# Performance work log

Measured on AMD Instinct MI355X. Metric: run time of the kernel, lower is better.

## Reference

```python
import jax, jax.numpy as jnp
import numpy as np

# Model config (matches init_kwargs)
V, SMAX, D, DH, H, M, L = 32000, 512, 512, 64, 8, 2048, 6
B, S, T = 4, 512, 512
PAD = 0

_SPEC = [
    ("tok_emb", (V, D), "n"), ("pos_emb", (SMAX, D), "n"),
    ("enc_ln1_w", (L, D), "1"), ("enc_ln1_b", (L, D), "0"),
    ("enc_wq", (L, H, D, DH), "n"), ("enc_wk", (L, H, D, DH), "n"), ("enc_wv", (L, H, D, DH), "n"),
    ("enc_wo", (L, H * DH, D), "n"), ("enc_bo", (L, D), "0"),
    ("enc_ln2_w", (L, D), "1"), ("enc_ln2_b", (L, D), "0"),
    ("enc_w1", (L, D, M), "n"), ("enc_b1", (L, M), "0"),
    ("enc_w2", (L, M, D), "n"), ("enc_b2", (L, D), "0"),
    ("enc_lnf_w", (D,), "1"), ("enc_lnf_b", (D,), "0"),
    ("dec_ln1_w", (L, D), "1"), ("dec_ln1_b", (L, D), "0"),
    ("dec_wq_s", (L, H, D, DH), "n"), ("dec_wk_s", (L, H, D, DH), "n"), ("dec_wv_s", (L, H, D, DH), "n"),
    ("dec_wo_s", (L, H * DH, D), "n"), ("dec_bo_s", (L, D), "0"),
    ("dec_ln2_w", (L, D), "1"), ("dec_ln2_b", (L, D), "0"),
    ("dec_wq_c", (L, H, D, DH), "n"), ("dec_wk_c", (L, H, D, DH), "n"), ("dec_wv_c", (L, H, D, DH), "n"),
    ("dec_wo_c", (L, H * DH, D), "n"), ("dec_bo_c", (L, D), "0"),
    ("dec_ln3_w", (L, D), "1"), ("dec_ln3_b", (L, D), "0"),
    ("dec_w1", (L, D, M), "n"), ("dec_b1", (L, M), "0"),
    ("dec_w2", (L, M, D), "n"), ("dec_b2", (L, D), "0"),
    ("dec_lnf_w", (D,), "1"), ("dec_lnf_b", (D,), "0"),
    ("head_w", (D, V), "n"), ("head_b", (V,), "0"),
]


def setup_inputs() -> dict:
    key = jax.random.key(0)
    k1, k2, key = jax.random.split(key, 3)
    inp = {
        "tokens_source": jax.random.randint(k1, (B, S), 0, V),
        "tokens_destination": jax.random.randint(k2, (B, T), 0, V),
    }
    for name, shape, kind in _SPEC:
        if kind == "n":
            key, k = jax.random.split(key)
            inp[name] = jax.random.normal(k, shape, jnp.float32) * 0.02
        elif kind == "1":
            inp[name] = jnp.ones(shape, jnp.float32)
        else:
            inp[name] = jnp.zeros(shape, jnp.float32)
    return inp


def _ln(x, w, b):
    mu = x.mean(-1, keepdims=True)
    var = ((x - mu) ** 2).mean(-1, keepdims=True)
    return (x - mu) * jax.lax.rsqrt(var + 1e-5) * w + b


def _mha(xq, xkv, wq, wk, wv, wo, bo, mask):
    # wq/wk/wv: [H, D, dh]; wo: [H*dh, D]; mask: bool [B or 1, Sq, Sk] (broadcast over heads)
    q = jnp.einsum("bsd,hde->bhse", xq, wq)
    k = jnp.einsum("btd,hde->bhte", xkv, wk)
    v = jnp.einsum("btd,hde->bhte", xkv, wv)
    scores = jnp.einsum("bhse,bhte->bhst", q, k) / (DH ** 0.5)
    scores = jnp.where(mask[:, None], scores, -jnp.inf)
    w = jax.nn.softmax(scores, axis=-1)
    o = jnp.einsum("bhst,bhte->bhse", w, v)
    b_, _, s_, _ = o.shape
    o = o.transpose(0, 2, 1, 3).reshape(b_, s_, H * DH)  # concat heads (head 0 first)
    return o @ wo + bo


def _forward(src, dst, p):
    s_, t_ = src.shape[1], dst.shape[1]
    key_mask = (src != PAD)[:, None, :]                      # [B,1,S]: mask over source keys
    causal = jnp.tril(jnp.ones((t_, t_), bool))[None]        # [1,T,T]
    x = p["tok_emb"][src] + p["pos_emb"][:s_]
    for i in range(L):
        h = _ln(x, p["enc_ln1_w"][i], p["enc_ln1_b"][i])
        x = x + _mha(h, h, p["enc_wq"][i], p["enc_wk"][i], p["enc_wv"][i], p["enc_wo"][i], p["enc_bo"][i], key_mask)
        h = _ln(x, p["enc_ln2_w"][i], p["enc_ln2_b"][i])
        x = x + jax.nn.gelu(h @ p["enc_w1"][i] + p["enc_b1"][i], approximate=False) @ p["enc_w2"][i] + p["enc_b2"][i]
    xe = _ln(x, p["enc_lnf_w"], p["enc_lnf_b"])
    y = p["tok_emb"][dst] + p["pos_emb"][:t_]
    for i in range(L):
        h = _ln(y, p["dec_ln1_w"][i], p["dec_ln1_b"][i])
        y = y + _mha(h, h, p["dec_wq_s"][i], p["dec_wk_s"][i], p["dec_wv_s"][i], p["dec_wo_s"][i], p["dec_bo_s"][i], causal)
        h = _ln(y, p["dec_ln2_w"][i], p["dec_ln2_b"][i])
        y = y + _mha(h, xe, p["dec_wq_c"][i], p["dec_wk_c"][i], p["dec_wv_c"][i], p["dec_wo_c"][i], p["dec_bo_c"][i], key_mask)
        h = _ln(y, p["dec_ln3_w"][i], p["dec_ln3_b"][i])
        y = y + jax.nn.gelu(h @ p["dec_w1"][i] + p["dec_b1"][i], approximate=False) @ p["dec_w2"][i] + p["dec_b2"][i]
    yd = _ln(y, p["dec_lnf_w"], p["dec_lnf_b"])
    return yd @ p["head_w"] + p["head_b"]  # logits [B, T, V]


def reference(tokens_source, tokens_destination, tok_emb, pos_emb, enc_ln1_w, enc_ln1_b, enc_wq, enc_wk, enc_wv, enc_wo, enc_bo, enc_ln2_w, enc_ln2_b, enc_w1, enc_b1, enc_w2, enc_b2, enc_lnf_w, enc_lnf_b, dec_ln1_w, dec_ln1_b, dec_wq_s, dec_wk_s, dec_wv_s, dec_wo_s, dec_bo_s, dec_ln2_w, dec_ln2_b, dec_wq_c, dec_wk_c, dec_wv_c, dec_wo_c, dec_bo_c, dec_ln3_w, dec_ln3_b, dec_w1, dec_b1, dec_w2, dec_b2, dec_lnf_w, dec_lnf_b, head_w, head_b):
    p = {k: v for k, v in locals().items() if k not in ("tokens_source", "tokens_destination")}
    return _forward(tokens_source, tokens_destination, p)
```

## Files before the change

### kernel.cpp

```cpp
#include <hip/hip_runtime.h>
#include <math.h>


typedef __bf16 bf16;
typedef bf16  bf16x8 __attribute__((ext_vector_type(8)));
typedef float f32x4  __attribute__((ext_vector_type(4)));

#define DEV __device__ __forceinline__

DEV f32x4 mfma16(bf16x8 a, bf16x8 b, f32x4 c) {
  return __builtin_amdgcn_mfma_f32_16x16x32_bf16(a, b, c, 0, 0, 0);
}

DEV void async_copy16(const bf16* g, bf16* l) {
  __builtin_amdgcn_global_load_lds(
      (__attribute__((address_space(1))) void*)(g),
      (__attribute__((address_space(3))) void*)(l), 16, 0, 0);
}

struct TJob { const float* in; bf16* out; long long oHi, oLo, oOfs; int R, C, zdiv, tile0; };
struct TJobs { TJob j[17]; };

__global__ __launch_bounds__(256) void tcast_all(TJobs JJ, int njobs)
{
  __shared__ float tile[32][33];
  const int t = blockIdx.x;
  int ji = 0;
#pragma unroll
  for (int k = 1; k < 17; ++k) if (k < njobs && JJ.j[k].tile0 <= t) ji = k;
  const TJob J = JJ.j[ji];
  const int rel  = t - J.tile0;
  const int ntx  = J.C >> 5, nty = J.R >> 5;
  const int perz = ntx * nty;
  const int z    = rel / perz;
  const int r2   = rel - z * perz;
  const int bx   = r2 % ntx, by = r2 / ntx;

  const long long zi = (long long)z * J.R * J.C;
  const long long zo = (long long)(z / J.zdiv) * J.oHi + (long long)(z % J.zdiv) * J.oLo + J.oOfs;
  const int c0 = bx * 32, r0 = by * 32;
  const int tx = threadIdx.x & 31, ty = (threadIdx.x >> 5);
#pragma unroll
  for (int i = 0; i < 32; i += 8)
    tile[ty + i][tx] = J.in[zi + (long long)(r0 + ty + i) * J.C + c0 + tx];
  __syncthreads();
#pragma unroll
  for (int i = 0; i < 32; i += 8)
    J.out[zo + (long long)(c0 + ty + i) * J.R + r0 + tx] = (bf16)tile[tx][ty + i];
}

__global__ __launch_bounds__(64) void embedln_kernel(
    const int* __restrict__ tok, const float* __restrict__ temb,
    const float* __restrict__ pemb, float* __restrict__ x,
    const float* __restrict__ w, const float* __restrict__ b,
    bf16* __restrict__ out)
{
  const int row  = blockIdx.x;
  const int sPos = row & 511;
  const int t    = tok[row];
  const int lane = threadIdx.x;
  const int c0   = lane * 8;
  f32x4 a0 = *(const f32x4*)&temb[(long long)t * 512 + c0];
  f32x4 a1 = *(const f32x4*)&temb[(long long)t * 512 + c0 + 4];
  f32x4 p0 = *(const f32x4*)&pemb[(long long)sPos * 512 + c0];
  f32x4 p1 = *(const f32x4*)&pemb[(long long)sPos * 512 + c0 + 4];
  a0 += p0; a1 += p1;
  *(f32x4*)&x[(long long)row * 512 + c0]     = a0;
  *(f32x4*)&x[(long long)row * 512 + c0 + 4] = a1;
  float s = 0.f, q = 0.f;
#pragma unroll
  for (int k = 0; k < 4; ++k) { s += a0[k] + a1[k]; q += a0[k]*a0[k] + a1[k]*a1[k]; }
#pragma unroll
  for (int m = 1; m < 64; m <<= 1) { s += __shfl_xor(s, m); q += __shfl_xor(q, m); }
  const float mean = s * (1.f / 512.f);
  const float var  = q * (1.f / 512.f) - mean * mean;
  const float rs   = rsqrtf(var + 1e-5f);
  f32x4 w0 = *(const f32x4*)&w[c0], w1 = *(const f32x4*)&w[c0 + 4];
  f32x4 b0 = *(const f32x4*)&b[c0], b1 = *(const f32x4*)&b[c0 + 4];
  bf16x8 o;
#pragma unroll
  for (int k = 0; k < 4; ++k) {
    o[k]     = (bf16)((a0[k] - mean) * rs * w0[k] + b0[k]);
    o[k + 4] = (bf16)((a1[k] - mean) * rs * w1[k] + b1[k]);
  }
  *(bf16x8*)&out[(long long)row * 512 + c0] = o;
}

__global__ __launch_bounds__(256) void addln_kernel(
    const bf16* __restrict__ g, const float* __restrict__ bias,
    float* __restrict__ x, const float* __restrict__ w,
    const float* __restrict__ bb, bf16* __restrict__ out)
{
  const int row  = blockIdx.x * 4 + (threadIdx.x >> 6);
  const int lane = threadIdx.x & 63;
  const int c0   = lane * 8;
  float* xr = x + (long long)row * 512;
  f32x4 a0 = *(const f32x4*)&xr[c0];
  f32x4 a1 = *(const f32x4*)&xr[c0 + 4];
  bf16x8 gv = *(const bf16x8*)&g[(long long)row * 512 + c0];
  f32x4 bi0 = *(const f32x4*)&bias[c0], bi1 = *(const f32x4*)&bias[c0 + 4];
  float v[8];
#pragma unroll
  for (int k = 0; k < 4; ++k) {
    v[k]     = a0[k] + (float)gv[k]     + bi0[k];
    v[k + 4] = a1[k] + (float)gv[k + 4] + bi1[k];
  }
  *(f32x4*)&xr[c0]     = f32x4{v[0], v[1], v[2], v[3]};
  *(f32x4*)&xr[c0 + 4] = f32x4{v[4], v[5], v[6], v[7]};
  float s = 0.f, q = 0.f;
#pragma unroll
  for (int k = 0; k < 8; ++k) { s += v[k]; q += v[k] * v[k]; }
#pragma unroll
  for (int m = 1; m < 64; m <<= 1) { s += __shfl_xor(s, m); q += __shfl_xor(q, m); }
  const float mean = s * (1.f / 512.f);
  const float var  = q * (1.f / 512.f) - mean * mean;
  const float rs   = rsqrtf(var + 1e-5f);
  f32x4 w0 = *(const f32x4*)&w[c0], w1 = *(const f32x4*)&w[c0 + 4];
  f32x4 b0 = *(const f32x4*)&bb[c0], b1 = *(const f32x4*)&bb[c0 + 4];
  bf16x8 o;
#pragma unroll
  for (int k = 0; k < 4; ++k) {
    o[k]     = (bf16)((v[k] - mean) * rs * w0[k] + b0[k]);
    o[k + 4] = (bf16)((v[k + 4] - mean) * rs * w1[k] + b1[k]);
  }
  *(bf16x8*)&out[(long long)row * 512 + c0] = o;
}

template <int MODE>
__global__ __launch_bounds__(64) void attn_kernel(
    const bf16* __restrict__ Q, const bf16* __restrict__ K,
    const bf16* __restrict__ Vt, bf16* __restrict__ O,
    const int* __restrict__ srctok)
{
  __shared__ bf16 Pw[16 * 68];
  const int bh = blockIdx.y;
  const int b  = bh >> 3;
  const int q0 = blockIdx.x * 16;
  const int ln = threadIdx.x;
  const int lr = ln & 15, g = ln >> 4;
  const bf16* Qg = Q + ((long long)bh * 512 + q0) * 64;
  const bf16* Kg = K + (long long)bh * 512 * 64;
  const bf16* Vg = Vt + (long long)bh * 64 * 512;
  const int* tkb = srctok + b * 512;

  const bf16x8 aq0 = *(const bf16x8*)&Qg[lr * 64 + g * 8];
  const bf16x8 aq1 = *(const bf16x8*)&Qg[lr * 64 + 32 + g * 8];

  float m[4] = {-1e30f, -1e30f, -1e30f, -1e30f};
  float l[4] = {0.f, 0.f, 0.f, 0.f};
  f32x4 o[4] = {};

  const int ktEnd = (MODE == 1) ? (q0 + 16) : 512;
  for (int kt = 0; kt < ktEnd; kt += 64) {
    f32x4 sf[4] = {};
#pragma unroll
    for (int j = 0; j < 4; ++j) {
      const bf16x8 bk0 = *(const bf16x8*)&Kg[(long long)(kt + j * 16 + lr) * 64 + g * 8];
      const bf16x8 bk1 = *(const bf16x8*)&Kg[(long long)(kt + j * 16 + lr) * 64 + 32 + g * 8];
      sf[j] = mfma16(aq0, bk0, sf[j]);
      sf[j] = mfma16(aq1, bk1, sf[j]);
    }
    float rm[4] = {-1e30f, -1e30f, -1e30f, -1e30f};
#pragma unroll
    for (int j = 0; j < 4; ++j) {
      if (MODE == 0) {
        const bool ok = (tkb[kt + j * 16 + lr] != 0);
#pragma unroll
        for (int r = 0; r < 4; ++r) if (!ok) sf[j][r] = -1e30f;
      } else {
        const int key = kt + j * 16 + lr;
#pragma unroll
        for (int r = 0; r < 4; ++r)
          if (key > q0 + g * 4 + r) sf[j][r] = -1e30f;
      }
#pragma unroll
      for (int r = 0; r < 4; ++r) rm[r] = fmaxf(rm[r], sf[j][r]);
    }
#pragma unroll
    for (int mk = 1; mk < 16; mk <<= 1)
#pragma unroll
      for (int r = 0; r < 4; ++r) rm[r] = fmaxf(rm[r], __shfl_xor(rm[r], mk));
    float al[4], ps[4] = {0.f, 0.f, 0.f, 0.f};
#pragma unroll
    for (int r = 0; r < 4; ++r) {
      const float mx = fmaxf(m[r], rm[r]);
      al[r] = __expf(m[r] - mx);
      m[r] = mx;
    }
#pragma unroll
    for (int j = 0; j < 4; ++j) {
#pragma unroll
      for (int r = 0; r < 4; ++r) {
        const float p = (sf[j][r] <= -1e29f) ? 0.f : __expf(sf[j][r] - m[r]);
        ps[r] += p;
        Pw[(g * 4 + r) * 68 + j * 16 + lr] = (bf16)p;
      }
    }
#pragma unroll
    for (int mk = 1; mk < 16; mk <<= 1)
#pragma unroll
      for (int r = 0; r < 4; ++r) ps[r] += __shfl_xor(ps[r], mk);
#pragma unroll
    for (int r = 0; r < 4; ++r) l[r] = l[r] * al[r] + ps[r];
#pragma unroll
    for (int n = 0; n < 4; ++n)
#pragma unroll
      for (int r = 0; r < 4; ++r) o[n][r] *= al[r];
#pragma unroll
    for (int ks = 0; ks < 2; ++ks) {
      const bf16x8 ap = *(const bf16x8*)&Pw[lr * 68 + ks * 32 + g * 8];
#pragma unroll
      for (int n = 0; n < 4; ++n) {
        const bf16x8 bv = *(const bf16x8*)&Vg[(long long)(n * 16 + lr) * 512 + kt + ks * 32 + g * 8];
        o[n] = mfma16(ap, bv, o[n]);
      }
    }
  }

#pragma unroll
  for (int r = 0; r < 4; ++r) {
    const float inv = 1.f / l[r];
    const long long gr = (long long)b * 512 + q0 + g * 4 + r;
#pragma unroll
    for (int n = 0; n < 4; ++n)
      O[gr * 512 + (bh & 7) * 64 + n * 16 + lr] = (bf16)(o[n][r] * inv);
  }
}

template <int BM, int BN, int EPI, bool SWZ = false>
__global__ __launch_bounds__(256) void gemm_kernel(
    const bf16* __restrict__ A, const bf16* __restrict__ Bw,
    void* __restrict__ Cc, const float* __restrict__ bias,
    const int K, const int lda, const int ldb, const int ldc,
    const long long sAz, const long long sBz,
    const long long sClo, const long long sChi, const int HB,
    const float scale)
{
  constexpr int BK = 64;
  __shared__ bf16 As[BM * BK];
  __shared__ bf16 Bs[BN * BK];
  constexpr int AISS = (BM * BK * 2) / 4096;
  constexpr int BISS = (BN * BK * 2) / 4096;

  const int z = blockIdx.z;
  const bf16* Az = A + (long long)z * sAz;
  const bf16* Bz = Bw + (long long)z * sBz;
  const long long cofs = (long long)(z % HB) * sClo + (long long)(z / HB) * sChi;

  const int tid  = threadIdx.x;
  const int wave = tid >> 6;
  const int lane = tid & 63;
  const int lr   = lane & 15;
  const int kg   = lane >> 4;

  int bx = blockIdx.x, by = blockIdx.y;
  if constexpr (SWZ) {
    const int nx = gridDim.x;
    const int nwg = nx * gridDim.y;
    const int id = by * nx + bx;
    const int chunk = nwg >> 3;
    const int swz = (id & 7) * chunk + (id >> 3);
    bx = swz % nx; by = swz / nx;
  }
  const int m0 = bx * BM;
  const int n0 = by * BN;

  constexpr int FM = BM / 32;
  constexpr int FN = BN / 32;
  const int wm = (wave >> 1) * (BM / 2);
  const int wn = (wave & 1) * (BN / 2);

  f32x4 acc[FM][FN] = {};

  for (int kt = 0; kt < K; kt += BK) {
#pragma unroll
    for (int i = 0; i < AISS; ++i) {
      const int o = i * 4096 + tid * 16;
      const int r = o >> 7;
      const int c = (o & 127) >> 1;
      async_copy16(Az + (long long)(m0 + r) * lda + kt + c, (bf16*)((char*)As + o));
    }
#pragma unroll
    for (int i = 0; i < BISS; ++i) {
      const int o = i * 4096 + tid * 16;
      const int r = o >> 7;
      const int c = (o & 127) >> 1;
      async_copy16(Bz + (long long)(n0 + r) * ldb + kt + c, (bf16*)((char*)Bs + o));
    }
    __syncthreads();
#pragma unroll
    for (int ks = 0; ks < 2; ++ks) {
      bf16x8 af[FM], bq[FN];
#pragma unroll
      for (int i = 0; i < FM; ++i)
        af[i] = *(const bf16x8*)&As[(wm + i * 16 + lr) * BK + ks * 32 + kg * 8];
#pragma unroll
      for (int j = 0; j < FN; ++j)
        bq[j] = *(const bf16x8*)&Bs[(wn + j * 16 + lr) * BK + ks * 32 + kg * 8];
#pragma unroll
      for (int i = 0; i < FM; ++i)
#pragma unroll
        for (int j = 0; j < FN; ++j)
          acc[i][j] = mfma16(af[i], bq[j], acc[i][j]);
    }
    __syncthreads();
  }

#pragma unroll
  for (int i = 0; i < FM; ++i) {
#pragma unroll
    for (int j = 0; j < FN; ++j) {
      const int gc = n0 + wn + j * 16 + lr;
#pragma unroll
      for (int r = 0; r < 4; ++r) {
        const int gr = m0 + wm + i * 16 + kg * 4 + r;
        const float v = acc[i][j][r];
        if constexpr (EPI == 0) {
          ((bf16*)Cc + cofs)[(long long)gr * ldc + gc] = (bf16)v;
        } else if constexpr (EPI == 3) {
          float t = v + bias[gc];
          t = 0.5f * t * (1.f + erff(t * 0.70710678118654752f));
          ((bf16*)Cc)[(long long)gr * ldc + gc] = (bf16)t;
        } else if constexpr (EPI == 4) {
          __builtin_nontemporal_store(v + bias[gc], &((float*)Cc)[(long long)gr * ldc + gc]);
        } else if constexpr (EPI == 7) {
          const int sel = gc >> 9;
          const int hh = (gc >> 6) & 7, ee = gc & 63;
          const int bb = gr >> 9, ss = gr & 511;
          bf16* base = (bf16*)Cc + (long long)sel * (2048 * 512);
          const float vv = (sel == 0) ? v * 0.125f : v;
          if (sel < 2) base[(((long long)(bb * 8 + hh) << 9) + ss) * 64 + ee] = (bf16)vv;
          else         base[(((long long)(bb * 8 + hh) << 6) + ee) * 512 + ss] = (bf16)vv;
        } else if constexpr (EPI == 8) {
          const int sel = gc >> 9;
          const int hh = (gc >> 6) & 7, ee = gc & 63;
          const int bb = gr >> 9, ss = gr & 511;
          bf16* base = (bf16*)Cc + (long long)z * sChi + (long long)sel * (2048 * 512);
          if (sel == 0) base[(((long long)(bb * 8 + hh) << 9) + ss) * 64 + ee] = (bf16)v;
          else          base[(((long long)(bb * 8 + hh) << 6) + ee) * 512 + ss] = (bf16)v;
        }
      }
    }
  }
}

extern "C" void kernel_launch(void* const* d_in, const int* in_sizes, int n_in,
                              void* d_out, int out_size, void* d_ws, size_t ws_size,
                              hipStream_t stream)
{
  const int*   tok_src   = (const int*)d_in[0];
  const int*   tok_dst   = (const int*)d_in[1];
  const float* tok_emb   = (const float*)d_in[2];
  const float* pos_emb   = (const float*)d_in[3];
  const float* enc_ln1_w = (const float*)d_in[4];
  const float* enc_ln1_b = (const float*)d_in[5];
  const float* enc_wq    = (const float*)d_in[6];
  const float* enc_wk    = (const float*)d_in[7];
  const float* enc_wv    = (const float*)d_in[8];
  const float* enc_wo    = (const float*)d_in[9];
  const float* enc_bo    = (const float*)d_in[10];
  const float* enc_ln2_w = (const float*)d_in[11];
  const float* enc_ln2_b = (const float*)d_in[12];
  const float* enc_w1    = (const float*)d_in[13];
  const float* enc_b1    = (const float*)d_in[14];
  const float* enc_w2    = (const float*)d_in[15];
  const float* enc_b2    = (const float*)d_in[16];
  const float* enc_lnf_w = (const float*)d_in[17];
  const float* enc_lnf_b = (const float*)d_in[18];
  const float* dec_ln1_w = (const float*)d_in[19];
  const float* dec_ln1_b = (const float*)d_in[20];
  const float* dec_wq_s  = (const float*)d_in[21];
  const float* dec_wk_s  = (const float*)d_in[22];
  const float* dec_wv_s  = (const float*)d_in[23];
  const float* dec_wo_s  = (const float*)d_in[24];
  const float* dec_bo_s  = (const float*)d_in[25];
  const float* dec_ln2_w = (const float*)d_in[26];
  const float* dec_ln2_b = (const float*)d_in[27];
  const float* dec_wq_c  = (const float*)d_in[28];
  const float* dec_wk_c  = (const float*)d_in[29];
  const float* dec_wv_c  = (const float*)d_in[30];
  const float* dec_wo_c  = (const float*)d_in[31];
  const float* dec_bo_c  = (const float*)d_in[32];
  const float* dec_ln3_w = (const float*)d_in[33];
  const float* dec_ln3_b = (const float*)d_in[34];
  const float* dec_w1    = (const float*)d_in[35];
  const float* dec_b1    = (const float*)d_in[36];
  const float* dec_w2    = (const float*)d_in[37];
  const float* dec_b2    = (const float*)d_in[38];
  const float* dec_lnf_w = (const float*)d_in[39];
  const float* dec_lnf_b = (const float*)d_in[40];
  const float* head_w    = (const float*)d_in[41];
  const float* head_b    = (const float*)d_in[42];
  float* outp = (float*)d_out;

  char* wp = (char*)d_ws;
  auto alloc = [&](size_t nbytes) -> char* {
    char* p = wp; wp += (nbytes + 255) & ~(size_t)255; return p;
  };
  const long long LQKV = 1536LL * 512;
  const long long LKV  = 1024LL * 512;
  const long long LSQ  = 512LL * 512;
  const long long LFF  = 2048LL * 512;
  const long long KVST = 2LL * 2048 * 512;

  bf16* tQKV_e = (bf16*)alloc((size_t)6 * LQKV * 2);
  bf16* tQKV_s = (bf16*)alloc((size_t)6 * LQKV * 2);
  bf16* tQ_c   = (bf16*)alloc((size_t)6 * LSQ * 2);
  bf16* tKV_c  = (bf16*)alloc((size_t)6 * LKV * 2);
  bf16* tWo_e  = (bf16*)alloc((size_t)6 * LSQ * 2);
  bf16* tWo_s  = (bf16*)alloc((size_t)6 * LSQ * 2);
  bf16* tWo_c  = (bf16*)alloc((size_t)6 * LSQ * 2);
  bf16* tW1_e  = (bf16*)alloc((size_t)6 * LFF * 2);
  bf16* tW2_e  = (bf16*)alloc((size_t)6 * LFF * 2);
  bf16* tW1_d  = (bf16*)alloc((size_t)6 * LFF * 2);
  bf16* tW2_d  = (bf16*)alloc((size_t)6 * LFF * 2);
  bf16* tHead  = (bf16*)alloc((size_t)32000 * 512 * 2);

  float* x   = (float*)alloc((size_t)2048 * 512 * 4);
  float* y   = (float*)alloc((size_t)2048 * 512 * 4);
  bf16*  h   = (bf16*)alloc((size_t)2048 * 512 * 2);
  bf16*  qkv = (bf16*)alloc((size_t)3 * 2048 * 512 * 2);
  bf16*  xe  = (bf16*)alloc((size_t)2048 * 512 * 2);
  bf16*  kvc = (bf16*)alloc((size_t)6 * KVST * 2);
  bf16*  ob  = (bf16*)alloc((size_t)2048 * 512 * 2);
  bf16*  t0  = (bf16*)alloc((size_t)2048 * 512 * 2);
  bf16*  h1  = (bf16*)alloc((size_t)2048 * 2048 * 2);
  bf16*  yd  = (bf16*)alloc((size_t)2048 * 512 * 2);

  bf16* ql = qkv;
  bf16* kl = qkv + 2048 * 512;
  bf16* vt = qkv + 2 * 2048 * 512;

  TJobs JJ; int nt = 0, nj = 0;
  auto addjob = [&](const float* in, bf16* out, int R, int C,
                    long long oHi, long long oLo, int zdiv, long long oOfs, int nz) {
    JJ.j[nj] = TJob{in, out, oHi, oLo, oOfs, R, C, zdiv, nt};
    nt += (C / 32) * (R / 32) * nz; ++nj;
  };
  addjob(enc_wq,   tQKV_e, 512, 64,   LQKV, 32768, 8, 0,      48);
  addjob(enc_wk,   tQKV_e, 512, 64,   LQKV, 32768, 8, 262144, 48);
  addjob(enc_wv,   tQKV_e, 512, 64,   LQKV, 32768, 8, 524288, 48);
  addjob(dec_wq_s, tQKV_s, 512, 64,   LQKV, 32768, 8, 0,      48);
  addjob(dec_wk_s, tQKV_s, 512, 64,   LQKV, 32768, 8, 262144, 48);
  addjob(dec_wv_s, tQKV_s, 512, 64,   LQKV, 32768, 8, 524288, 48);
  addjob(dec_wq_c, tQ_c,   512, 64,   LSQ,  32768, 8, 0,      48);
  addjob(dec_wk_c, tKV_c,  512, 64,   LKV,  32768, 8, 0,      48);
  addjob(dec_wv_c, tKV_c,  512, 64,   LKV,  32768, 8, 262144, 48);
  addjob(enc_wo,   tWo_e,  512, 512,  LSQ,  0, 1, 0, 6);
  addjob(dec_wo_s, tWo_s,  512, 512,  LSQ,  0, 1, 0, 6);
  addjob(dec_wo_c, tWo_c,  512, 512,  LSQ,  0, 1, 0, 6);
  addjob(enc_w1,   tW1_e,  512, 2048, LFF,  0, 1, 0, 6);
  addjob(enc_w2,   tW2_e,  2048, 512, LFF,  0, 1, 0, 6);
  addjob(dec_w1,   tW1_d,  512, 2048, LFF,  0, 1, 0, 6);
  addjob(dec_w2,   tW2_d,  2048, 512, LFF,  0, 1, 0, 6);
  addjob(head_w,   tHead,  512, 32000, 0,   0, 1, 0, 1);
  tcast_all<<<nt, 256, 0, stream>>>(JJ, nj);

  embedln_kernel<<<2048, 64, 0, stream>>>(tok_src, tok_emb, pos_emb, x, enc_ln1_w, enc_ln1_b, h);
  for (int l = 0; l < 6; ++l) {
    gemm_kernel<128, 128, 7><<<dim3(16, 12, 1), 256, 0, stream>>>(
        h, tQKV_e + (size_t)l * LQKV, qkv, nullptr, 512, 512, 512, 0, 0, 0, 0, 0, 1, 1.f);
    attn_kernel<0><<<dim3(32, 32), 64, 0, stream>>>(ql, kl, vt, ob, tok_src);
    gemm_kernel<64, 64, 0><<<dim3(32, 8, 1), 256, 0, stream>>>(
        ob, tWo_e + (size_t)l * LSQ, t0, nullptr, 512, 512, 512, 512, 0, 0, 0, 0, 1, 1.f);
    addln_kernel<<<512, 256, 0, stream>>>(t0, enc_bo + l * 512, x,
        enc_ln2_w + l * 512, enc_ln2_b + l * 512, h);
    gemm_kernel<128, 128, 3><<<dim3(16, 16, 1), 256, 0, stream>>>(
        h, tW1_e + (size_t)l * LFF, h1, enc_b1 + l * 2048, 512, 512, 512, 2048, 0, 0, 0, 0, 1, 1.f);
    gemm_kernel<64, 64, 0><<<dim3(32, 8, 1), 256, 0, stream>>>(
        h1, tW2_e + (size_t)l * LFF, t0, nullptr, 2048, 2048, 2048, 512, 0, 0, 0, 0, 1, 1.f);
    const float* nw = (l < 5) ? enc_ln1_w + (l + 1) * 512 : enc_lnf_w;
    const float* nb = (l < 5) ? enc_ln1_b + (l + 1) * 512 : enc_lnf_b;
    addln_kernel<<<512, 256, 0, stream>>>(t0, enc_b2 + l * 512, x, nw, nb, (l < 5) ? h : xe);
  }

  gemm_kernel<128, 128, 8><<<dim3(16, 8, 6), 256, 0, stream>>>(
      xe, tKV_c, kvc, nullptr, 512, 512, 512, 0, 0, LKV, 0, KVST, 1, 1.f);

  embedln_kernel<<<2048, 64, 0, stream>>>(tok_dst, tok_emb, pos_emb, y, dec_ln1_w, dec_ln1_b, h);
  for (int l = 0; l < 6; ++l) {
    gemm_kernel<128, 128, 7><<<dim3(16, 12, 1), 256, 0, stream>>>(
        h, tQKV_s + (size_t)l * LQKV, qkv, nullptr, 512, 512, 512, 0, 0, 0, 0, 0, 1, 1.f);
    attn_kernel<1><<<dim3(32, 32), 64, 0, stream>>>(ql, kl, vt, ob, nullptr);
    gemm_kernel<64, 64, 0><<<dim3(32, 8, 1), 256, 0, stream>>>(
        ob, tWo_s + (size_t)l * LSQ, t0, nullptr, 512, 512, 512, 512, 0, 0, 0, 0, 1, 1.f);
    addln_kernel<<<512, 256, 0, stream>>>(t0, dec_bo_s + l * 512, y,
        dec_ln2_w + l * 512, dec_ln2_b + l * 512, h);
    gemm_kernel<64, 64, 7><<<dim3(32, 8, 1), 256, 0, stream>>>(
        h, tQ_c + (size_t)l * LSQ, qkv, nullptr, 512, 512, 512, 0, 0, 0, 0, 0, 1, 1.f);
    attn_kernel<0><<<dim3(32, 32), 64, 0, stream>>>(
        ql, kvc + (size_t)l * KVST, kvc + (size_t)l * KVST + 2048 * 512, ob, tok_src);
    gemm_kernel<64, 64, 0><<<dim3(32, 8, 1), 256, 0, stream>>>(
        ob, tWo_c + (size_t)l * LSQ, t0, nullptr, 512, 512, 512, 512, 0, 0, 0, 0, 1, 1.f);
    addln_kernel<<<512, 256, 0, stream>>>(t0, dec_bo_c + l * 512, y,
        dec_ln3_w + l * 512, dec_ln3_b + l * 512, h);
    gemm_kernel<128, 128, 3><<<dim3(16, 16, 1), 256, 0, stream>>>(
        h, tW1_d + (size_t)l * LFF, h1, dec_b1 + l * 2048, 512, 512, 512, 2048, 0, 0, 0, 0, 1, 1.f);
    gemm_kernel<64, 64, 0><<<dim3(32, 8, 1), 256, 0, stream>>>(
        h1, tW2_d + (size_t)l * LFF, t0, nullptr, 2048, 2048, 2048, 512, 0, 0, 0, 0, 1, 1.f);
    const float* nw = (l < 5) ? dec_ln1_w + (l + 1) * 512 : dec_lnf_w;
    const float* nb = (l < 5) ? dec_ln1_b + (l + 1) * 512 : dec_lnf_b;
    addln_kernel<<<512, 256, 0, stream>>>(t0, dec_b2 + l * 512, y, nw, nb, (l < 5) ? h : yd);
  }
  gemm_kernel<128, 128, 4, true><<<dim3(16, 250, 1), 256, 0, stream>>>(
      yd, tHead, outp, head_b, 512, 512, 512, 32000, 0, 0, 0, 0, 1, 1.f);
}
```

Baseline: 2.252 ms.

## Double-buffer GEMM LDS tiles, hoist attention K/V loads, shrink QKV/FFN1 tiles

```diff
diff --git a/kernel.cpp b/kernel.cpp
--- a/kernel.cpp
+++ b/kernel.cpp
@@ -152,13 +152,22 @@
 
   const int ktEnd = (MODE == 1) ? (q0 + 16) : 512;
   for (int kt = 0; kt < ktEnd; kt += 64) {
+    bf16x8 bk[4][2], bv[4][2];
+#pragma unroll
+    for (int j = 0; j < 4; ++j) {
+      bk[j][0] = *(const bf16x8*)&Kg[(long long)(kt + j * 16 + lr) * 64 + g * 8];
+      bk[j][1] = *(const bf16x8*)&Kg[(long long)(kt + j * 16 + lr) * 64 + 32 + g * 8];
+    }
+#pragma unroll
+    for (int n = 0; n < 4; ++n) {
+      bv[n][0] = *(const bf16x8*)&Vg[(long long)(n * 16 + lr) * 512 + kt + g * 8];
+      bv[n][1] = *(const bf16x8*)&Vg[(long long)(n * 16 + lr) * 512 + kt + 32 + g * 8];
+    }
     f32x4 sf[4] = {};
 #pragma unroll
     for (int j = 0; j < 4; ++j) {
-      const bf16x8 bk0 = *(const bf16x8*)&Kg[(long long)(kt + j * 16 + lr) * 64 + g * 8];
-      const bf16x8 bk1 = *(const bf16x8*)&Kg[(long long)(kt + j * 16 + lr) * 64 + 32 + g * 8];
-      sf[j] = mfma16(aq0, bk0, sf[j]);
-      sf[j] = mfma16(aq1, bk1, sf[j]);
+      sf[j] = mfma16(aq0, bk[j][0], sf[j]);
+      sf[j] = mfma16(aq1, bk[j][1], sf[j]);
     }
     float rm[4] = {-1e30f, -1e30f, -1e30f, -1e30f};
 #pragma unroll
@@ -210,10 +219,8 @@
     for (int ks = 0; ks < 2; ++ks) {
       const bf16x8 ap = *(const bf16x8*)&Pw[lr * 68 + ks * 32 + g * 8];
 #pragma unroll
-      for (int n = 0; n < 4; ++n) {
-        const bf16x8 bv = *(const bf16x8*)&Vg[(long long)(n * 16 + lr) * 512 + kt + ks * 32 + g * 8];
-        o[n] = mfma16(ap, bv, o[n]);
-      }
+      for (int n = 0; n < 4; ++n)
+        o[n] = mfma16(ap, bv[n][ks], o[n]);
     }
   }
 
@@ -237,8 +244,8 @@
     const float scale)
 {
   constexpr int BK = 64;
-  __shared__ bf16 As[BM * BK];
-  __shared__ bf16 Bs[BN * BK];
+  __shared__ bf16 As[2][BM * BK];
+  __shared__ bf16 Bs[2][BN * BK];
   constexpr int AISS = (BM * BK * 2) / 4096;
   constexpr int BISS = (BN * BK * 2) / 4096;
 
@@ -272,38 +279,53 @@
 
   f32x4 acc[FM][FN] = {};
 
-  for (int kt = 0; kt < K; kt += BK) {
+  auto stage = [&](int buf, int kt) {
 #pragma unroll
     for (int i = 0; i < AISS; ++i) {
       const int o = i * 4096 + tid * 16;
       const int r = o >> 7;
       const int c = (o & 127) >> 1;
-      async_copy16(Az + (long long)(m0 + r) * lda + kt + c, (bf16*)((char*)As + o));
+      async_copy16(Az + (long long)(m0 + r) * lda + kt + c, (bf16*)((char*)&As[buf][0] + o));
     }
 #pragma unroll
     for (int i = 0; i < BISS; ++i) {
       const int o = i * 4096 + tid * 16;
       const int r = o >> 7;
       const int c = (o & 127) >> 1;
-      async_copy16(Bz + (long long)(n0 + r) * ldb + kt + c, (bf16*)((char*)Bs + o));
-    }
-    __syncthreads();
+      async_copy16(Bz + (long long)(n0 + r) * ldb + kt + c, (bf16*)((char*)&Bs[buf][0] + o));
+    }
+  };
+
+  const int NT = K / BK;
+  stage(0, 0);
+  asm volatile("s_waitcnt vmcnt(0)" ::: "memory");
+  __builtin_amdgcn_s_barrier();
+  __builtin_amdgcn_sched_barrier(0);
+
+  int cur = 0;
+  for (int t = 0; t < NT; ++t) {
+    if (t + 1 < NT) stage(cur ^ 1, (t + 1) * BK);
 #pragma unroll
     for (int ks = 0; ks < 2; ++ks) {
       bf16x8 af[FM], bq[FN];
 #pragma unroll
       for (int i = 0; i < FM; ++i)
-        af[i] = *(const bf16x8*)&As[(wm + i * 16 + lr) * BK + ks * 32 + kg * 8];
+        af[i] = *(const bf16x8*)&As[cur][(wm + i * 16 + lr) * BK + ks * 32 + kg * 8];
 #pragma unroll
       for (int j = 0; j < FN; ++j)
-        bq[j] = *(const bf16x8*)&Bs[(wn + j * 16 + lr) * BK + ks * 32 + kg * 8];
+        bq[j] = *(const bf16x8*)&Bs[cur][(wn + j * 16 + lr) * BK + ks * 32 + kg * 8];
 #pragma unroll
       for (int i = 0; i < FM; ++i)
 #pragma unroll
         for (int j = 0; j < FN; ++j)
           acc[i][j] = mfma16(af[i], bq[j], acc[i][j]);
     }
-    __syncthreads();
+    if (t + 1 < NT) {
+      asm volatile("s_waitcnt vmcnt(0) lgkmcnt(0)" ::: "memory");
+      __builtin_amdgcn_s_barrier();
+      __builtin_amdgcn_sched_barrier(0);
+      cur ^= 1;
+    }
   }
 
 #pragma unroll
@@ -458,14 +480,14 @@
 
   embedln_kernel<<<2048, 64, 0, stream>>>(tok_src, tok_emb, pos_emb, x, enc_ln1_w, enc_ln1_b, h);
   for (int l = 0; l < 6; ++l) {
-    gemm_kernel<128, 128, 7><<<dim3(16, 12, 1), 256, 0, stream>>>(
+    gemm_kernel<64, 128, 7><<<dim3(32, 12, 1), 256, 0, stream>>>(
         h, tQKV_e + (size_t)l * LQKV, qkv, nullptr, 512, 512, 512, 0, 0, 0, 0, 0, 1, 1.f);
     attn_kernel<0><<<dim3(32, 32), 64, 0, stream>>>(ql, kl, vt, ob, tok_src);
     gemm_kernel<64, 64, 0><<<dim3(32, 8, 1), 256, 0, stream>>>(
         ob, tWo_e + (size_t)l * LSQ, t0, nullptr, 512, 512, 512, 512, 0, 0, 0, 0, 1, 1.f);
     addln_kernel<<<512, 256, 0, stream>>>(t0, enc_bo + l * 512, x,
         enc_ln2_w + l * 512, enc_ln2_b + l * 512, h);
-    gemm_kernel<128, 128, 3><<<dim3(16, 16, 1), 256, 0, stream>>>(
+    gemm_kernel<64, 128, 3><<<dim3(32, 16, 1), 256, 0, stream>>>(
         h, tW1_e + (size_t)l * LFF, h1, enc_b1 + l * 2048, 512, 512, 512, 2048, 0, 0, 0, 0, 1, 1.f);
     gemm_kernel<64, 64, 0><<<dim3(32, 8, 1), 256, 0, stream>>>(
         h1, tW2_e + (size_t)l * LFF, t0, nullptr, 2048, 2048, 2048, 512, 0, 0, 0, 0, 1, 1.f);
@@ -479,7 +501,7 @@
 
   embedln_kernel<<<2048, 64, 0, stream>>>(tok_dst, tok_emb, pos_emb, y, dec_ln1_w, dec_ln1_b, h);
   for (int l = 0; l < 6; ++l) {
-    gemm_kernel<128, 128, 7><<<dim3(16, 12, 1), 256, 0, stream>>>(
+    gemm_kernel<64, 128, 7><<<dim3(32, 12, 1), 256, 0, stream>>>(
         h, tQKV_s + (size_t)l * LQKV, qkv, nullptr, 512, 512, 512, 0, 0, 0, 0, 0, 1, 1.f);
     attn_kernel<1><<<dim3(32, 32), 64, 0, stream>>>(ql, kl, vt, ob, nullptr);
     gemm_kernel<64, 64, 0><<<dim3(32, 8, 1), 256, 0, stream>>>(
@@ -494,7 +516,7 @@
         ob, tWo_c + (size_t)l * LSQ, t0, nullptr, 512, 512, 512, 512, 0, 0, 0, 0, 1, 1.f);
     addln_kernel<<<512, 256, 0, stream>>>(t0, dec_bo_c + l * 512, y,
         dec_ln3_w + l * 512, dec_ln3_b + l * 512, h);
-    gemm_kernel<128, 128, 3><<<dim3(16, 16, 1), 256, 0, stream>>>(
+    gemm_kernel<64, 128, 3><<<dim3(32, 16, 1), 256, 0, stream>>>(
         h, tW1_d + (size_t)l * LFF, h1, dec_b1 + l * 2048, 512, 512, 512, 2048, 0, 0, 0, 0, 1, 1.f);
     gemm_kernel<64, 64, 0><<<dim3(32, 8, 1), 256, 0, stream>>>(
         h1, tW2_d + (size_t)l * LFF, t0, nullptr, 2048, 2048, 2048, 512, 0, 0, 0, 0, 1, 1.f);
```

New measurement: 2.144 ms. -4.8%, faster.
